# Kernel optimization log

Hardware: AMD Instinct MI355X
Metric: run time of the kernel (lower is better)

## Reference

```python
import jax, jax.numpy as jnp
import numpy as np

H = 1024
B = 32
T = 2048


def setup_inputs() -> dict:
    key = jax.random.key(0)
    k1, k2, k3, k4, k5, k6 = jax.random.split(key, 6)
    hidden = jax.random.normal(k1, (B, H), dtype=jnp.float32)
    encoder_outputs = jax.random.normal(k2, (T, B, H), dtype=jnp.float32)  # [T,B,H]
    processed_location = jax.random.normal(k3, (B, T, H), dtype=jnp.float32)
    mask = jax.random.randint(k4, (B, T), 0, 2, dtype=jnp.int32)
    # learned params: processed_query Linear(H,H,bias=False), attn Linear(H,1,bias=False)
    scale = 1.0 / np.sqrt(H)
    Wq = jax.random.uniform(k5, (H, H), dtype=jnp.float32, minval=-scale, maxval=scale)
    Wa = jax.random.uniform(k6, (1, H), dtype=jnp.float32, minval=-scale, maxval=scale)
    return {"hidden": hidden, "encoder_outputs": encoder_outputs,
            "processed_location": processed_location, "mask": mask,
            "Wq": Wq, "Wa": Wa}


def reference(hidden, encoder_outputs, processed_location, mask, Wq, Wa):
    # 'general' method of Attn
    enc = jnp.swapaxes(encoder_outputs, 0, 1)           # [B,T,H]
    q = jax.nn.relu(hidden @ Wq.T)                      # [B,H]
    content = jnp.einsum('bth,bh->bt', enc, q)[..., None]  # [B,T,1]
    energy = jnp.tanh(content + processed_location) @ Wa.T  # [B,T,1]
    energies = energy[..., 0]                            # [B,T]
    energies = jnp.where(mask.astype(bool), -jnp.inf, energies)
    attn = jax.nn.softmax(energies, axis=1)[:, None, :]  # [B,1,T]
    return attn, energies
```

## Files before the change

### kernel.cpp

```cpp
#include <hip/hip_runtime.h>
#include <math.h>

#define H 1024
#define B 32
#define T 2048

#define MASKED_ENERGY (-1.0e30f)

__device__ __forceinline__ float wave_reduce_sum(float v) {
    v += __shfl_xor(v, 32);
    v += __shfl_xor(v, 16);
    v += __shfl_xor(v, 8);
    v += __shfl_xor(v, 4);
    v += __shfl_xor(v, 2);
    v += __shfl_xor(v, 1);
    return v;
}

__device__ __forceinline__ float fast_tanh(float x) {
    float cx = fminf(fmaxf(x, -10.0f), 10.0f);
    float e  = __expf(2.0f * cx);
    return (e - 1.0f) * __builtin_amdgcn_rcpf(e + 1.0f);
}

__global__ void qk_kernel(const float* __restrict__ hidden,
                          const float* __restrict__ Wq,
                          float* __restrict__ q) {
    const int lane = threadIdx.x & 63;
    const int wid  = threadIdx.x >> 6;
    const int i    = blockIdx.x * 4 + wid;
    const int b    = blockIdx.y;
    const float4* wrow = (const float4*)(Wq + (size_t)i * H);
    const float4* hrow = (const float4*)(hidden + (size_t)b * H);
    float s = 0.f;
#pragma unroll
    for (int c = 0; c < 4; ++c) {
        float4 w = wrow[lane + c * 64];
        float4 h = hrow[lane + c * 64];
        s += w.x * h.x + w.y * h.y + w.z * h.z + w.w * h.w;
    }
    s = wave_reduce_sum(s);
    if (lane == 0) q[(size_t)b * H + i] = fmaxf(s, 0.f);
}

__global__ void energy_kernel(const float* __restrict__ enc,
                              const float* __restrict__ pl,
                              const int*   __restrict__ mask,
                              const float* __restrict__ q,
                              const float* __restrict__ Wa,
                              float* __restrict__ energies) {
    const int lane = threadIdx.x & 63;
    const int wid  = threadIdx.x >> 6;
    const int p    = blockIdx.x * 4 + wid;
    const int b    = p >> 11;
    const int t    = p & (T - 1);

    if (mask[p]) {
        if (lane == 0) energies[p] = MASKED_ENERGY;
        return;
    }

    const float4* ep = (const float4*)(enc + ((size_t)t * B + b) * H);
    const float4* pp = (const float4*)(pl  + ((size_t)b * T + t) * H);
    const float4* qp = (const float4*)(q   + (size_t)b * H);
    const float4* wp = (const float4*)Wa;

    float4 ev[4], pv[4], qv[4], wv[4];
#pragma unroll
    for (int c = 0; c < 4; ++c) {
        const int idx = lane + c * 64;
        ev[c] = ep[idx];
        qv[c] = qp[idx];
        pv[c] = pp[idx];
        wv[c] = wp[idx];
    }

    float cs = 0.f;
#pragma unroll
    for (int c = 0; c < 4; ++c)
        cs += ev[c].x * qv[c].x + ev[c].y * qv[c].y +
              ev[c].z * qv[c].z + ev[c].w * qv[c].w;
    const float content = wave_reduce_sum(cs);

    float es = 0.f;
#pragma unroll
    for (int c = 0; c < 4; ++c) {
        es += wv[c].x * fast_tanh(content + pv[c].x);
        es += wv[c].y * fast_tanh(content + pv[c].y);
        es += wv[c].z * fast_tanh(content + pv[c].z);
        es += wv[c].w * fast_tanh(content + pv[c].w);
    }
    es = wave_reduce_sum(es);
    if (lane == 0) energies[p] = es;
}

__global__ void softmax_kernel(const float* __restrict__ energies,
                               float* __restrict__ attn) {
    const int b   = blockIdx.x;
    const int tid = threadIdx.x;
    __shared__ float red[256];
    const float* e = energies + (size_t)b * T;

    float ev[8];
    float m = -INFINITY;
#pragma unroll
    for (int k = 0; k < 8; ++k) {
        ev[k] = e[tid + k * 256];
        m = fmaxf(m, ev[k]);
    }
    red[tid] = m;
    __syncthreads();
    for (int s = 128; s > 0; s >>= 1) {
        if (tid < s) red[tid] = fmaxf(red[tid], red[tid + s]);
        __syncthreads();
    }
    const float maxv = red[0];
    __syncthreads();

    float sum = 0.f;
    float ex[8];
#pragma unroll
    for (int k = 0; k < 8; ++k) {
        ex[k] = __expf(ev[k] - maxv);
        sum += ex[k];
    }
    red[tid] = sum;
    __syncthreads();
    for (int s = 128; s > 0; s >>= 1) {
        if (tid < s) red[tid] += red[tid + s];
        __syncthreads();
    }
    const float inv = 1.0f / red[0];
#pragma unroll
    for (int k = 0; k < 8; ++k)
        attn[(size_t)b * T + tid + k * 256] = ex[k] * inv;
}

extern "C" void kernel_launch(void* const* d_in, const int* in_sizes, int n_in,
                              void* d_out, int out_size, void* d_ws, size_t ws_size,
                              hipStream_t stream) {
    const float* hidden = (const float*)d_in[0];
    const float* enc    = (const float*)d_in[1];
    const float* pl     = (const float*)d_in[2];
    const int*   mask   = (const int*)d_in[3];
    const float* Wq     = (const float*)d_in[4];
    const float* Wa     = (const float*)d_in[5];

    float* out      = (float*)d_out;
    float* attn     = out;
    float* energies = out + (size_t)B * T;
    float* qws      = (float*)d_ws;

    qk_kernel<<<dim3(H / 4, B), 256, 0, stream>>>(hidden, Wq, qws);
    energy_kernel<<<dim3(B * T / 4), 256, 0, stream>>>(enc, pl, mask, qws, Wa, energies);
    softmax_kernel<<<dim3(B), 256, 0, stream>>>(energies, attn);
}
```

Before: 480.8 us.

## Reuse Wq rows across batches, stream inputs nontemporally, simplify tanh and softmax reductions

The query kernel now keeps each Wq row in registers and computes 16 batch rows per wave, which cuts redundant weight reads and the grid size. The energy kernel uses nontemporal loads for the large encoder and location streams and computes tanh as 1-2/(e^{2x}+1) with no clamping. The softmax kernel replaces the shared-memory tree reductions with wave shuffles plus a 4-entry combine. Risks: with no clamp, very large |x| relies on exp overflowing to inf and rcp returning 0 to give the correct limit, and the qk grid now exposes much less parallelism.

```diff
diff --git a/kernel.cpp b/kernel.cpp
--- a/kernel.cpp
+++ b/kernel.cpp
@@ -6,6 +6,8 @@
 #define T 2048
 
 #define MASKED_ENERGY (-1.0e30f)
+
+typedef float f4 __attribute__((ext_vector_type(4)));
 
 __device__ __forceinline__ float wave_reduce_sum(float v) {
     v += __shfl_xor(v, 32);
@@ -17,10 +19,20 @@
     return v;
 }
 
-__device__ __forceinline__ float fast_tanh(float x) {
-    float cx = fminf(fmaxf(x, -10.0f), 10.0f);
-    float e  = __expf(2.0f * cx);
-    return (e - 1.0f) * __builtin_amdgcn_rcpf(e + 1.0f);
+__device__ __forceinline__ float wave_reduce_max(float v) {
+    v = fmaxf(v, __shfl_xor(v, 32));
+    v = fmaxf(v, __shfl_xor(v, 16));
+    v = fmaxf(v, __shfl_xor(v, 8));
+    v = fmaxf(v, __shfl_xor(v, 4));
+    v = fmaxf(v, __shfl_xor(v, 2));
+    v = fmaxf(v, __shfl_xor(v, 1));
+    return v;
+}
+
+__device__ __forceinline__ float tanh_term(float w, float x, float acc) {
+    const float e = __expf(2.0f * x);
+    const float r = __builtin_amdgcn_rcpf(e + 1.0f);
+    return fmaf(w, 1.0f - (r + r), acc);
 }
 
 __global__ void qk_kernel(const float* __restrict__ hidden,
@@ -29,18 +41,29 @@
     const int lane = threadIdx.x & 63;
     const int wid  = threadIdx.x >> 6;
     const int i    = blockIdx.x * 4 + wid;
-    const int b    = blockIdx.y;
-    const float4* wrow = (const float4*)(Wq + (size_t)i * H);
-    const float4* hrow = (const float4*)(hidden + (size_t)b * H);
-    float s = 0.f;
+    const int b0   = blockIdx.y * 16;
+    const f4* wrow = (const f4*)(Wq + (size_t)i * H);
+
+    f4 w[4];
 #pragma unroll
-    for (int c = 0; c < 4; ++c) {
-        float4 w = wrow[lane + c * 64];
-        float4 h = hrow[lane + c * 64];
-        s += w.x * h.x + w.y * h.y + w.z * h.z + w.w * h.w;
+    for (int c = 0; c < 4; ++c) w[c] = wrow[lane + c * 64];
+
+#pragma unroll
+    for (int bb = 0; bb < 16; ++bb) {
+        const int b = b0 + bb;
+        const f4* hrow = (const f4*)(hidden + (size_t)b * H);
+        float s = 0.f;
+#pragma unroll
+        for (int c = 0; c < 4; ++c) {
+            f4 h = hrow[lane + c * 64];
+            s = fmaf(w[c].x, h.x, s);
+            s = fmaf(w[c].y, h.y, s);
+            s = fmaf(w[c].z, h.z, s);
+            s = fmaf(w[c].w, h.w, s);
+        }
+        s = wave_reduce_sum(s);
+        if (lane == 0) q[(size_t)b * H + i] = fmaxf(s, 0.f);
     }
-    s = wave_reduce_sum(s);
-    if (lane == 0) q[(size_t)b * H + i] = fmaxf(s, 0.f);
 }
 
 __global__ void energy_kernel(const float* __restrict__ enc,
@@ -60,35 +83,38 @@
         return;
     }
 
-    const float4* ep = (const float4*)(enc + ((size_t)t * B + b) * H);
-    const float4* pp = (const float4*)(pl  + ((size_t)b * T + t) * H);
-    const float4* qp = (const float4*)(q   + (size_t)b * H);
-    const float4* wp = (const float4*)Wa;
+    const f4* ep = (const f4*)(enc + ((size_t)t * B + b) * H);
+    const f4* pp = (const f4*)(pl  + ((size_t)b * T + t) * H);
+    const f4* qp = (const f4*)(q   + (size_t)b * H);
+    const f4* wp = (const f4*)Wa;
 
-    float4 ev[4], pv[4], qv[4], wv[4];
+    f4 ev[4], pv[4], qv[4], wv[4];
 #pragma unroll
     for (int c = 0; c < 4; ++c) {
         const int idx = lane + c * 64;
-        ev[c] = ep[idx];
+        ev[c] = __builtin_nontemporal_load(ep + idx);
+        pv[c] = __builtin_nontemporal_load(pp + idx);
         qv[c] = qp[idx];
-        pv[c] = pp[idx];
         wv[c] = wp[idx];
     }
 
     float cs = 0.f;
 #pragma unroll
-    for (int c = 0; c < 4; ++c)
-        cs += ev[c].x * qv[c].x + ev[c].y * qv[c].y +
-              ev[c].z * qv[c].z + ev[c].w * qv[c].w;
+    for (int c = 0; c < 4; ++c) {
+        cs = fmaf(ev[c].x, qv[c].x, cs);
+        cs = fmaf(ev[c].y, qv[c].y, cs);
+        cs = fmaf(ev[c].z, qv[c].z, cs);
+        cs = fmaf(ev[c].w, qv[c].w, cs);
+    }
     const float content = wave_reduce_sum(cs);
 
     float es = 0.f;
 #pragma unroll
     for (int c = 0; c < 4; ++c) {
-        es += wv[c].x * fast_tanh(content + pv[c].x);
-        es += wv[c].y * fast_tanh(content + pv[c].y);
-        es += wv[c].z * fast_tanh(content + pv[c].z);
-        es += wv[c].w * fast_tanh(content + pv[c].w);
+        es = tanh_term(wv[c].x, content + pv[c].x, es);
+        es = tanh_term(wv[c].y, content + pv[c].y, es);
+        es = tanh_term(wv[c].z, content + pv[c].z, es);
+        es = tanh_term(wv[c].w, content + pv[c].w, es);
     }
     es = wave_reduce_sum(es);
     if (lane == 0) energies[p] = es;
@@ -96,9 +122,12 @@
 
 __global__ void softmax_kernel(const float* __restrict__ energies,
                                float* __restrict__ attn) {
-    const int b   = blockIdx.x;
-    const int tid = threadIdx.x;
-    __shared__ float red[256];
+    const int b    = blockIdx.x;
+    const int tid  = threadIdx.x;
+    const int lane = tid & 63;
+    const int wid  = tid >> 6;
+    __shared__ float redm[4];
+    __shared__ float reds[4];
     const float* e = energies + (size_t)b * T;
 
     float ev[8];
@@ -108,29 +137,22 @@
         ev[k] = e[tid + k * 256];
         m = fmaxf(m, ev[k]);
     }
-    red[tid] = m;
+    m = wave_reduce_max(m);
+    if (lane == 0) redm[wid] = m;
     __syncthreads();
-    for (int s = 128; s > 0; s >>= 1) {
-        if (tid < s) red[tid] = fmaxf(red[tid], red[tid + s]);
-        __syncthreads();
-    }
-    const float maxv = red[0];
-    __syncthreads();
+    const float maxv = fmaxf(fmaxf(redm[0], redm[1]), fmaxf(redm[2], redm[3]));
 
+    float ex[8];
     float sum = 0.f;
-    float ex[8];
 #pragma unroll
     for (int k = 0; k < 8; ++k) {
         ex[k] = __expf(ev[k] - maxv);
         sum += ex[k];
     }
-    red[tid] = sum;
+    sum = wave_reduce_sum(sum);
+    if (lane == 0) reds[wid] = sum;
     __syncthreads();
-    for (int s = 128; s > 0; s >>= 1) {
-        if (tid < s) red[tid] += red[tid + s];
-        __syncthreads();
-    }
-    const float inv = 1.0f / red[0];
+    const float inv = 1.0f / (reds[0] + reds[1] + reds[2] + reds[3]);
 #pragma unroll
     for (int k = 0; k < 8; ++k)
         attn[(size_t)b * T + tid + k * 256] = ex[k] * inv;
@@ -151,7 +173,7 @@
     float* energies = out + (size_t)B * T;
     float* qws      = (float*)d_ws;
 
-    qk_kernel<<<dim3(H / 4, B), 256, 0, stream>>>(hidden, Wq, qws);
+    qk_kernel<<<dim3(H / 4, 2), 256, 0, stream>>>(hidden, Wq, qws);
     energy_kernel<<<dim3(B * T / 4), 256, 0, stream>>>(enc, pl, mask, qws, Wa, energies);
     softmax_kernel<<<dim3(B), 256, 0, stream>>>(energies, attn);
 }
```

New measurement: 459.7 us. 1.05x faster.
